# Optimization experiments

Hardware: AMD Instinct MI355X
Metric: run time of the kernel (lower is better)

Reference implementation:

```python
import jax, jax.numpy as jnp
import numpy as np

EPS = 1e-8  # torch.cosine_similarity eps


def setup_inputs() -> dict:
    key = jax.random.key(0)
    k1, k2 = jax.random.split(key)
    N, D, TOPIC_E, NT = 4096, 512, 10, 6  # NT = topic_e - topic_s + 1
    x = jax.random.normal(k1, (N, D), dtype=jnp.float32)
    # H mimics the concatenated, abs()'d H_list: (input_feature, topic_e, num_topics)
    H = jax.random.uniform(k2, (D, TOPIC_E, NT), dtype=jnp.float32)
    return {"x": x, "H": H}


def reference(x, H):
    N, D = x.shape
    num_topics = H.shape[2]

    # W_list[n, t, i] = (x @ H[:, :, i])[n, t]
    W_list = jnp.einsum('nd,dti->nti', x, H)          # (N, topic_e, num_topics)
    W_max = jnp.argmax(W_list, axis=1)                # (N, num_topics), int

    # cosine similarity matrix S[a, b] = cos(x[a], x[b]) (symmetric)
    norms = jnp.maximum(jnp.linalg.norm(x, axis=1), EPS)  # (N,)
    xn = x / norms[:, None]
    S = xn @ xn.T                                      # (N, N)

    # topic-match fraction F[a, b] = mean_k [W_max[a,k] == W_max[b,k]] (symmetric)
    comp = (W_max[:, None, :] == W_max[None, :, :])    # (N, N, num_topics) bool
    F = comp.sum(axis=2).astype(jnp.float32) / num_topics

    # C[a, b] = topic_count * sim; new_nodes[b] = mean_a C[a,b] * cat(x[b], x[a])
    C = F * S                                          # (N, N)
    col_mean = C.mean(axis=0)                          # (N,) mean over a
    out_first = x * col_mean[:, None]                  # (N, D): x[b] * mean_a C[a,b]
    out_second = (C.T @ x) / N                         # (N, D): (1/N) sum_a C[a,b] x[a]
    return jnp.concatenate([out_first, out_second], axis=1)  # (N, 2D)
```

## Files before the change

### kernel.cpp

```cpp
#include <hip/hip_runtime.h>
#include <hip/hip_bf16.h>

#define DD 512
#define NTOP 10
#define NTK 6
#define NPAIR 60

typedef float f32x4 __attribute__((ext_vector_type(4)));
typedef short bf16x8 __attribute__((ext_vector_type(8)));
typedef unsigned short us8 __attribute__((ext_vector_type(8)));
typedef unsigned short us4 __attribute__((ext_vector_type(4)));

__device__ __forceinline__ void gload16(const void* g, void* l) {
  __builtin_amdgcn_global_load_lds(
      (const __attribute__((address_space(1))) unsigned int*)g,
      (__attribute__((address_space(3))) unsigned int*)l, 16, 0, 0);
}

__global__ __launch_bounds__(256) void kern_wmax(
    const float* __restrict__ x, const float* __restrict__ H,
    int* __restrict__ codes, float* __restrict__ inv_norm,
    float* __restrict__ col_sum)
{
  __shared__ float xs[4][DD];
  __shared__ float w[4][NPAIR];
  const int wv = threadIdx.x >> 6, lane = threadIdx.x & 63;
  const int n = blockIdx.x * 4 + wv;
  const float* xr = x + (size_t)n * DD;
  float ss = 0.f;
#pragma unroll
  for (int j = 0; j < 2; ++j) {
    float4 v = *(const float4*)(xr + j * 256 + lane * 4);
    *(float4*)&xs[wv][j * 256 + lane * 4] = v;
    ss = fmaf(v.x, v.x, fmaf(v.y, v.y, fmaf(v.z, v.z, fmaf(v.w, v.w, ss))));
  }
#pragma unroll
  for (int off = 32; off; off >>= 1) ss += __shfl_xor(ss, off);
  if (lane == 0) inv_norm[n] = 1.0f / fmaxf(sqrtf(ss), 1e-8f);
  __syncthreads();
  if (lane < NPAIR) {
    float acc = 0.f;
#pragma unroll 8
    for (int d = 0; d < DD; ++d) acc = fmaf(xs[wv][d], H[d * NPAIR + lane], acc);
    w[wv][lane] = acc;
  }
  __syncthreads();
  int myc = 0;
  if (lane < NTK) {
    float best = w[wv][lane];
    int bi = 0;
#pragma unroll
    for (int t = 1; t < NTOP; ++t) {
      float v = w[wv][t * NTK + lane];
      if (v > best) { best = v; bi = t; }
    }
    myc = bi << (4 * lane);
  }
#pragma unroll
  for (int off = 1; off <= 4; off <<= 1) myc |= __shfl_xor(myc, off);
  if (lane == 0) { codes[n] = myc; col_sum[n] = 0.f; }
}

__global__ __launch_bounds__(256) void kern_prep(
    const float* __restrict__ x, const float* __restrict__ inv_norm,
    __hip_bfloat16* __restrict__ xn, __hip_bfloat16* __restrict__ xT, int N)
{
  __shared__ float tile[64][65];
  const int n0 = blockIdx.x * 64, d0 = blockIdx.y * 64;
  const int tid = threadIdx.x;
  const int r = tid >> 2, cseg = (tid & 3) * 16;
  const float* src = x + (size_t)(n0 + r) * DD + d0 + cseg;
  const float invn = inv_norm[n0 + r];
  unsigned short hb[16];
#pragma unroll
  for (int q = 0; q < 4; ++q) {
    float4 v = *(const float4*)(src + q * 4);
    tile[r][cseg + q * 4 + 0] = v.x; tile[r][cseg + q * 4 + 1] = v.y;
    tile[r][cseg + q * 4 + 2] = v.z; tile[r][cseg + q * 4 + 3] = v.w;
    hb[q * 4 + 0] = __builtin_bit_cast(unsigned short, __float2bfloat16(v.x * invn));
    hb[q * 4 + 1] = __builtin_bit_cast(unsigned short, __float2bfloat16(v.y * invn));
    hb[q * 4 + 2] = __builtin_bit_cast(unsigned short, __float2bfloat16(v.z * invn));
    hb[q * 4 + 3] = __builtin_bit_cast(unsigned short, __float2bfloat16(v.w * invn));
  }
  us8 v0, v1;
#pragma unroll
  for (int i = 0; i < 8; ++i) { v0[i] = hb[i]; v1[i] = hb[i + 8]; }
  *(us8*)(xn + (size_t)(n0 + r) * DD + d0 + cseg) = v0;
  *(us8*)(xn + (size_t)(n0 + r) * DD + d0 + cseg + 8) = v1;
  __syncthreads();
  const int drow = tid >> 2, nseg = (tid & 3) * 16;
  unsigned short hb2[16];
#pragma unroll
  for (int i = 0; i < 16; ++i)
    hb2[i] = __builtin_bit_cast(unsigned short, __float2bfloat16(tile[nseg + i][drow]));
  us8 w0, w1;
#pragma unroll
  for (int i = 0; i < 8; ++i) { w0[i] = hb2[i]; w1[i] = hb2[i + 8]; }
  *(us8*)(xT + (size_t)(d0 + drow) * N + n0 + nseg) = w0;
  *(us8*)(xT + (size_t)(d0 + drow) * N + n0 + nseg + 8) = w1;
}

#define GBM 128
#define GBK 64

__global__ __launch_bounds__(512, 4) void kern_gram(
    const __hip_bfloat16* __restrict__ xn, const int* __restrict__ codes,
    __hip_bfloat16* __restrict__ Cb, float* __restrict__ col_sum, int N)
{
  __shared__ __hip_bfloat16 lds[2 * GBM * GBK];
  __shared__ float csA[GBM], csB[GBM];
  __hip_bfloat16* As = lds;
  __hip_bfloat16* Bs = lds + GBM * GBK;
  const int tid = threadIdx.x;

  int idx = blockIdx.x, ai = 0, rem = N / GBM;
  while (idx >= rem) { idx -= rem; ++ai; --rem; }
  const int bi = ai + idx;
  const bool diag = (ai == bi);
  const int a0 = ai * GBM, b0 = bi * GBM;

  if (tid < GBM) { csA[tid] = 0.f; csB[tid] = 0.f; }

  const int lane = tid & 63, wid = tid >> 6;
  const int wr = wid >> 2, wc = wid & 3;

  const f32x4 fz = {0.f, 0.f, 0.f, 0.f};
  f32x4 acc[4][2];
#pragma unroll
  for (int m = 0; m < 4; ++m)
#pragma unroll
    for (int n = 0; n < 2; ++n) acc[m][n] = fz;

  int ldsoff[2]; size_t srcA[2], srcB[2];
#pragma unroll
  for (int i = 0; i < 2; ++i) {
    int p = i * 8192 + tid * 16;
    int row = p >> 7, c = (p >> 4) & 7;
    ldsoff[i] = p;
    size_t cc = (size_t)((c ^ (row & 7)) << 4);
    srcA[i] = (size_t)(a0 + row) * (DD * 2) + cc;
    srcB[i] = (size_t)(b0 + row) * (DD * 2) + cc;
  }
  const char* xc = (const char*)xn;

  for (int kc = 0; kc < DD * 2; kc += GBK * 2) {
#pragma unroll
    for (int i = 0; i < 2; ++i) {
      gload16(xc + srcA[i] + kc, (char*)As + ldsoff[i]);
      gload16(xc + srcB[i] + kc, (char*)Bs + ldsoff[i]);
    }
    __syncthreads();
#pragma unroll
    for (int kk = 0; kk < 2; ++kk) {
      const int kb = kk * 64 + (lane >> 4) * 16;
      bf16x8 af[4], bfr[2];
#pragma unroll
      for (int m = 0; m < 4; ++m) {
        int r = wr * 64 + m * 16 + (lane & 15);
        af[m] = *(const bf16x8*)((const char*)As + r * 128 + (kb ^ ((r & 7) << 4)));
      }
#pragma unroll
      for (int n = 0; n < 2; ++n) {
        int r = wc * 32 + n * 16 + (lane & 15);
        bfr[n] = *(const bf16x8*)((const char*)Bs + r * 128 + (kb ^ ((r & 7) << 4)));
      }
#pragma unroll
      for (int m = 0; m < 4; ++m)
#pragma unroll
        for (int n = 0; n < 2; ++n)
          acc[m][n] = __builtin_amdgcn_mfma_f32_16x16x32_bf16(af[m], bfr[n], acc[m][n], 0, 0, 0);
    }
    __syncthreads();
  }

  char* ldsb = (char*)lds;
  const int rq = (lane >> 4) << 2;
  int cb[2];
#pragma unroll
  for (int n = 0; n < 2; ++n) cb[n] = codes[b0 + wc * 32 + n * 16 + (lane & 15)];

  us4 tvs[4][2];
  float colpart[2] = {0.f, 0.f};
  float rowpart[4][4] = {};
#pragma unroll
  for (int m = 0; m < 4; ++m) {
    int ca[4];
#pragma unroll
    for (int j = 0; j < 4; ++j) ca[j] = codes[a0 + wr * 64 + m * 16 + rq + j];
#pragma unroll
    for (int n = 0; n < 2; ++n) {
      const int col = wc * 32 + n * 16 + (lane & 15);
#pragma unroll
      for (int j = 0; j < 4; ++j) {
        int t = ca[j] ^ cb[n];
        t |= t >> 1; t |= t >> 2;
        t &= 0x111111;
        float f = (float)(6 - __popc(t)) * (1.0f / 6.0f);
        float cv = acc[m][n][j] * f;
        colpart[n] += cv;
        rowpart[m][j] += cv;
        __hip_bfloat16 hv = __float2bfloat16(cv);
        tvs[m][n][j] = __builtin_bit_cast(unsigned short, hv);
        const int row = wr * 64 + m * 16 + rq + j;
        const int boff = row * 256 + ((((col >> 3) ^ (row & 7)) << 4) | ((col & 7) << 1));
        *(__hip_bfloat16*)(ldsb + boff) = hv;
      }
    }
  }
#pragma unroll
  for (int n = 0; n < 2; ++n) {
    float v = colpart[n];
    v += __shfl_xor(v, 16);
    v += __shfl_xor(v, 32);
    if (lane < 16) atomicAdd(&csB[wc * 32 + n * 16 + lane], v);
  }
  if (!diag) {
#pragma unroll
    for (int m = 0; m < 4; ++m)
#pragma unroll
      for (int j = 0; j < 4; ++j) {
        float v = rowpart[m][j];
        v += __shfl_xor(v, 1);
        v += __shfl_xor(v, 2);
        v += __shfl_xor(v, 4);
        v += __shfl_xor(v, 8);
        if ((lane & 15) == 0)
          atomicAdd(&csA[wr * 64 + m * 16 + rq + j], v);
      }
  }
  __syncthreads();
#pragma unroll
  for (int i = 0; i < 4; ++i) {
    const int row = i * 32 + (tid >> 4);
    const int ch = tid & 15;
    us8 v = *(us8*)(ldsb + row * 256 + ((ch ^ (row & 7)) << 4));
    *(us8*)((char*)Cb + ((size_t)(a0 + row) * N + b0) * 2 + (ch << 4)) = v;
  }
  if (!diag) {
    __syncthreads();
#pragma unroll
    for (int m = 0; m < 4; ++m) {
      const int row0 = wr * 64 + m * 16 + rq;
      const int chT = row0 >> 3;
      const int byo = (row0 & 7) << 1;
#pragma unroll
      for (int n = 0; n < 2; ++n) {
        const int col = wc * 32 + n * 16 + (lane & 15);
        *(us4*)(ldsb + col * 256 + (((chT ^ (col & 7)) << 4) | byo)) = tvs[m][n];
      }
    }
    __syncthreads();
#pragma unroll
    for (int i = 0; i < 4; ++i) {
      const int row = i * 32 + (tid >> 4);
      const int ch = tid & 15;
      us8 v = *(us8*)(ldsb + row * 256 + ((ch ^ (row & 7)) << 4));
      *(us8*)((char*)Cb + ((size_t)(b0 + row) * N + a0) * 2 + (ch << 4)) = v;
    }
  }
  if (tid < GBM) {
    atomicAdd(&col_sum[b0 + tid], csB[tid]);
    if (!diag) atomicAdd(&col_sum[a0 + tid], csA[tid]);
  }
}

#define OM 128
#define ON 128
#define OK 64
#define OSK 4

__global__ __launch_bounds__(512, 4) void kern_out2(
    const __hip_bfloat16* __restrict__ Cb, const __hip_bfloat16* __restrict__ xT,
    float* __restrict__ part, int N)
{
  __shared__ __hip_bfloat16 As[OM * OK];
  __shared__ __hip_bfloat16 Bs[ON * OK];
  const int tid = threadIdx.x;
  const int b0 = blockIdx.x * OM;
  const int d0 = blockIdx.y * ON;
  const int KSL = N / OSK;
  const size_t kbyte0 = (size_t)blockIdx.z * KSL * 2;
  const int lane = tid & 63, wid = tid >> 6;
  const int wr = wid >> 2, wc = wid & 3;

  const f32x4 fz = {0.f, 0.f, 0.f, 0.f};
  f32x4 acc[4][2];
#pragma unroll
  for (int m = 0; m < 4; ++m)
#pragma unroll
    for (int n = 0; n < 2; ++n) acc[m][n] = fz;

  int ldso[2]; size_t srcA[2], srcB[2];
#pragma unroll
  for (int i = 0; i < 2; ++i) {
    int p = i * 8192 + tid * 16;
    int row = p >> 7, c = (p >> 4) & 7;
    ldso[i] = p;
    size_t cc = (size_t)((c ^ (row & 7)) << 4);
    srcA[i] = (size_t)(b0 + row) * ((size_t)N * 2) + cc + kbyte0;
    srcB[i] = (size_t)(d0 + row) * ((size_t)N * 2) + cc + kbyte0;
  }
  const char* Ac = (const char*)Cb;
  const char* Bc = (const char*)xT;

  for (int kc = 0; kc < KSL * 2; kc += OK * 2) {
#pragma unroll
    for (int i = 0; i < 2; ++i) {
      gload16(Ac + srcA[i] + kc, (char*)As + ldso[i]);
      gload16(Bc + srcB[i] + kc, (char*)Bs + ldso[i]);
    }
    __syncthreads();
#pragma unroll
    for (int kk = 0; kk < 2; ++kk) {
      const int kb = kk * 64 + (lane >> 4) * 16;
      bf16x8 af[4], bfr[2];
#pragma unroll
      for (int m = 0; m < 4; ++m) {
        int r = wr * 64 + m * 16 + (lane & 15);
        af[m] = *(const bf16x8*)((const char*)As + r * 128 + (kb ^ ((r & 7) << 4)));
      }
#pragma unroll
      for (int n = 0; n < 2; ++n) {
        int r = wc * 32 + n * 16 + (lane & 15);
        bfr[n] = *(const bf16x8*)((const char*)Bs + r * 128 + (kb ^ ((r & 7) << 4)));
      }
#pragma unroll
      for (int m = 0; m < 4; ++m)
#pragma unroll
        for (int n = 0; n < 2; ++n)
          acc[m][n] = __builtin_amdgcn_mfma_f32_16x16x32_bf16(af[m], bfr[n], acc[m][n], 0, 0, 0);
    }
    __syncthreads();
  }

  float* pz = part + (size_t)blockIdx.z * N * DD;
#pragma unroll
  for (int m = 0; m < 4; ++m)
#pragma unroll
    for (int j = 0; j < 4; ++j) {
      int b = b0 + wr * 64 + m * 16 + ((lane >> 4) << 2) + j;
#pragma unroll
      for (int n = 0; n < 2; ++n) {
        int d = d0 + wc * 32 + n * 16 + (lane & 15);
        pz[(size_t)b * DD + d] = acc[m][n][j];
      }
    }
}

__global__ __launch_bounds__(256) void kern_finish(
    const float* __restrict__ x, const float* __restrict__ col_sum,
    const float* __restrict__ part, float* __restrict__ out, int N)
{
  const int n = blockIdx.x;
  const int tid = threadIdx.x;
  const float invN = 1.0f / (float)N;
  if (tid < 128) {
    const float s = col_sum[n] * invN;
    float4 v = ((const float4*)(x + (size_t)n * DD))[tid];
    v.x *= s; v.y *= s; v.z *= s; v.w *= s;
    ((float4*)(out + (size_t)n * (2 * DD)))[tid] = v;
  } else {
    const int d4 = tid - 128;
    const size_t stride = (size_t)N * DD;
    const float4* p0 = (const float4*)(part + (size_t)n * DD) + d4;
    const float4* p1 = (const float4*)(part + stride + (size_t)n * DD) + d4;
    const float4* p2 = (const float4*)(part + 2 * stride + (size_t)n * DD) + d4;
    const float4* p3 = (const float4*)(part + 3 * stride + (size_t)n * DD) + d4;
    float4 a = *p0, b = *p1, c = *p2, d = *p3;
    float4 r;
    r.x = ((a.x + b.x) + (c.x + d.x)) * invN;
    r.y = ((a.y + b.y) + (c.y + d.y)) * invN;
    r.z = ((a.z + b.z) + (c.z + d.z)) * invN;
    r.w = ((a.w + b.w) + (c.w + d.w)) * invN;
    ((float4*)(out + (size_t)n * (2 * DD) + DD))[d4] = r;
  }
}

extern "C" void kernel_launch(void* const* d_in, const int* in_sizes, int n_in,
                              void* d_out, int out_size, void* d_ws, size_t ws_size,
                              hipStream_t stream) {
  const float* x = (const float*)d_in[0];
  const float* H = (const float*)d_in[1];
  float* out = (float*)d_out;
  const int N = in_sizes[0] / DD;

  char* ws = (char*)d_ws;
  __hip_bfloat16* Cb   = (__hip_bfloat16*)ws;
  __hip_bfloat16* xn16 = (__hip_bfloat16*)(ws + (size_t)N * N * 2);
  __hip_bfloat16* xT16 = xn16 + (size_t)N * DD;
  float* part     = (float*)(xT16 + (size_t)N * DD);
  float* col_sum  = part + (size_t)4 * N * DD;
  float* inv_norm = col_sum + N;
  int*   codes    = (int*)(inv_norm + N);

  kern_wmax<<<N / 4, 256, 0, stream>>>(x, H, codes, inv_norm, col_sum);
  kern_prep<<<dim3(N / 64, DD / 64), 256, 0, stream>>>(x, inv_norm, xn16, xT16, N);
  const int T = N / GBM;
  kern_gram<<<T * (T + 1) / 2, 512, 0, stream>>>(xn16, codes, Cb, col_sum, N);
  kern_out2<<<dim3(N / OM, DD / ON, OSK), 512, 0, stream>>>(Cb, xT16, part, N);
  kern_finish<<<N, 256, 0, stream>>>(x, col_sum, part, out, N);
}
```

Before: 87.69 us.

## Widen out2 GEMM tile to 128x256 with 8-way split-K and reorder gram blocks

Adds a second C^T·x GEMM kernel that uses 128x256 output tiles, so each loaded Cb tile is reused across twice as many columns. It splits K eight ways to keep the grid large and falls back to the old 128x128, 4-way split when the workspace is too small for eight partial buffers. The gram kernel now schedules off-diagonal tiles before the cheaper diagonal tiles. The cost is twice as much partial-sum traffic in the finish kernel and more accumulator registers per thread.

```diff
diff --git a/kernel.cpp b/kernel.cpp
--- a/kernel.cpp
+++ b/kernel.cpp
@@ -113,9 +113,16 @@
   __hip_bfloat16* Bs = lds + GBM * GBK;
   const int tid = threadIdx.x;
 
-  int idx = blockIdx.x, ai = 0, rem = N / GBM;
-  while (idx >= rem) { idx -= rem; ++ai; --rem; }
-  const int bi = ai + idx;
+  const int T = N / GBM;
+  const int NOFF = T * (T - 1) / 2;
+  int ai, bi;
+  if ((int)blockIdx.x < NOFF) {
+    int idx = blockIdx.x; ai = 0; int rem = T - 1;
+    while (idx >= rem) { idx -= rem; ++ai; --rem; }
+    bi = ai + 1 + idx;
+  } else {
+    ai = bi = blockIdx.x - NOFF;
+  }
   const bool diag = (ai == bi);
   const int a0 = ai * GBM, b0 = bi * GBM;
 
@@ -264,21 +271,99 @@
   }
 }
 
-#define OM 128
-#define ON 128
-#define OK 64
-#define OSK 4
-
-__global__ __launch_bounds__(512, 4) void kern_out2(
+__global__ __launch_bounds__(512, 4) void kern_out2b(
     const __hip_bfloat16* __restrict__ Cb, const __hip_bfloat16* __restrict__ xT,
     float* __restrict__ part, int N)
 {
-  __shared__ __hip_bfloat16 As[OM * OK];
-  __shared__ __hip_bfloat16 Bs[ON * OK];
+  __shared__ __hip_bfloat16 As[128 * 64];
+  __shared__ __hip_bfloat16 Bs[256 * 64];
   const int tid = threadIdx.x;
-  const int b0 = blockIdx.x * OM;
-  const int d0 = blockIdx.y * ON;
-  const int KSL = N / OSK;
+  const int b0 = blockIdx.x * 128;
+  const int d0 = blockIdx.y * 256;
+  const int KSL = N / 8;
+  const size_t kbyte0 = (size_t)blockIdx.z * KSL * 2;
+  const int lane = tid & 63, wid = tid >> 6;
+  const int wr = wid >> 2, wc = wid & 3;
+
+  const f32x4 fz = {0.f, 0.f, 0.f, 0.f};
+  f32x4 acc[4][4];
+#pragma unroll
+  for (int m = 0; m < 4; ++m)
+#pragma unroll
+    for (int n = 0; n < 4; ++n) acc[m][n] = fz;
+
+  int ldsA[2]; size_t srcA[2];
+#pragma unroll
+  for (int i = 0; i < 2; ++i) {
+    int p = i * 8192 + tid * 16;
+    int row = p >> 7, c = (p >> 4) & 7;
+    ldsA[i] = p;
+    srcA[i] = (size_t)(b0 + row) * ((size_t)N * 2) + (size_t)((c ^ (row & 7)) << 4) + kbyte0;
+  }
+  int ldsB[4]; size_t srcB[4];
+#pragma unroll
+  for (int i = 0; i < 4; ++i) {
+    int p = i * 8192 + tid * 16;
+    int row = p >> 7, c = (p >> 4) & 7;
+    ldsB[i] = p;
+    srcB[i] = (size_t)(d0 + row) * ((size_t)N * 2) + (size_t)((c ^ (row & 7)) << 4) + kbyte0;
+  }
+  const char* Ac = (const char*)Cb;
+  const char* Bc = (const char*)xT;
+
+  for (int kc = 0; kc < KSL * 2; kc += 128) {
+#pragma unroll
+    for (int i = 0; i < 2; ++i) gload16(Ac + srcA[i] + kc, (char*)As + ldsA[i]);
+#pragma unroll
+    for (int i = 0; i < 4; ++i) gload16(Bc + srcB[i] + kc, (char*)Bs + ldsB[i]);
+    __syncthreads();
+#pragma unroll
+    for (int kk = 0; kk < 2; ++kk) {
+      const int kb = kk * 64 + (lane >> 4) * 16;
+      bf16x8 af[4], bfr[4];
+#pragma unroll
+      for (int m = 0; m < 4; ++m) {
+        int r = wr * 64 + m * 16 + (lane & 15);
+        af[m] = *(const bf16x8*)((const char*)As + r * 128 + (kb ^ ((r & 7) << 4)));
+      }
+#pragma unroll
+      for (int n = 0; n < 4; ++n) {
+        int r = wc * 64 + n * 16 + (lane & 15);
+        bfr[n] = *(const bf16x8*)((const char*)Bs + r * 128 + (kb ^ ((r & 7) << 4)));
+      }
+#pragma unroll
+      for (int m = 0; m < 4; ++m)
+#pragma unroll
+        for (int n = 0; n < 4; ++n)
+          acc[m][n] = __builtin_amdgcn_mfma_f32_16x16x32_bf16(af[m], bfr[n], acc[m][n], 0, 0, 0);
+    }
+    __syncthreads();
+  }
+
+  float* pz = part + (size_t)blockIdx.z * N * DD;
+#pragma unroll
+  for (int m = 0; m < 4; ++m)
+#pragma unroll
+    for (int j = 0; j < 4; ++j) {
+      int b = b0 + wr * 64 + m * 16 + ((lane >> 4) << 2) + j;
+#pragma unroll
+      for (int n = 0; n < 4; ++n) {
+        int d = d0 + wc * 64 + n * 16 + (lane & 15);
+        pz[(size_t)b * DD + d] = acc[m][n][j];
+      }
+    }
+}
+
+__global__ __launch_bounds__(512, 4) void kern_out2f(
+    const __hip_bfloat16* __restrict__ Cb, const __hip_bfloat16* __restrict__ xT,
+    float* __restrict__ part, int N)
+{
+  __shared__ __hip_bfloat16 As[128 * 64];
+  __shared__ __hip_bfloat16 Bs[128 * 64];
+  const int tid = threadIdx.x;
+  const int b0 = blockIdx.x * 128;
+  const int d0 = blockIdx.y * 128;
+  const int KSL = N / 4;
   const size_t kbyte0 = (size_t)blockIdx.z * KSL * 2;
   const int lane = tid & 63, wid = tid >> 6;
   const int wr = wid >> 2, wc = wid & 3;
@@ -303,7 +388,7 @@
   const char* Ac = (const char*)Cb;
   const char* Bc = (const char*)xT;
 
-  for (int kc = 0; kc < KSL * 2; kc += OK * 2) {
+  for (int kc = 0; kc < KSL * 2; kc += 128) {
 #pragma unroll
     for (int i = 0; i < 2; ++i) {
       gload16(Ac + srcA[i] + kc, (char*)As + ldso[i]);
@@ -349,7 +434,7 @@
 
 __global__ __launch_bounds__(256) void kern_finish(
     const float* __restrict__ x, const float* __restrict__ col_sum,
-    const float* __restrict__ part, float* __restrict__ out, int N)
+    const float* __restrict__ part, float* __restrict__ out, int N, int osk)
 {
   const int n = blockIdx.x;
   const int tid = threadIdx.x;
@@ -362,16 +447,12 @@
   } else {
     const int d4 = tid - 128;
     const size_t stride = (size_t)N * DD;
-    const float4* p0 = (const float4*)(part + (size_t)n * DD) + d4;
-    const float4* p1 = (const float4*)(part + stride + (size_t)n * DD) + d4;
-    const float4* p2 = (const float4*)(part + 2 * stride + (size_t)n * DD) + d4;
-    const float4* p3 = (const float4*)(part + 3 * stride + (size_t)n * DD) + d4;
-    float4 a = *p0, b = *p1, c = *p2, d = *p3;
-    float4 r;
-    r.x = ((a.x + b.x) + (c.x + d.x)) * invN;
-    r.y = ((a.y + b.y) + (c.y + d.y)) * invN;
-    r.z = ((a.z + b.z) + (c.z + d.z)) * invN;
-    r.w = ((a.w + b.w) + (c.w + d.w)) * invN;
+    float4 r = {0.f, 0.f, 0.f, 0.f};
+    for (int z = 0; z < osk; ++z) {
+      float4 p = *((const float4*)(part + (size_t)z * stride + (size_t)n * DD) + d4);
+      r.x += p.x; r.y += p.y; r.z += p.z; r.w += p.w;
+    }
+    r.x *= invN; r.y *= invN; r.z *= invN; r.w *= invN;
     ((float4*)(out + (size_t)n * (2 * DD) + DD))[d4] = r;
   }
 }
@@ -388,15 +469,23 @@
   __hip_bfloat16* Cb   = (__hip_bfloat16*)ws;
   __hip_bfloat16* xn16 = (__hip_bfloat16*)(ws + (size_t)N * N * 2);
   __hip_bfloat16* xT16 = xn16 + (size_t)N * DD;
-  float* part     = (float*)(xT16 + (size_t)N * DD);
-  float* col_sum  = part + (size_t)4 * N * DD;
+  float* col_sum  = (float*)(xT16 + (size_t)N * DD);
   float* inv_norm = col_sum + N;
   int*   codes    = (int*)(inv_norm + N);
+  float* part     = (float*)(codes + N);
+
+  const size_t base = (size_t)((char*)part - ws);
+  const bool big = ws_size >= base + (size_t)8 * N * DD * sizeof(float);
 
   kern_wmax<<<N / 4, 256, 0, stream>>>(x, H, codes, inv_norm, col_sum);
   kern_prep<<<dim3(N / 64, DD / 64), 256, 0, stream>>>(x, inv_norm, xn16, xT16, N);
   const int T = N / GBM;
   kern_gram<<<T * (T + 1) / 2, 512, 0, stream>>>(xn16, codes, Cb, col_sum, N);
-  kern_out2<<<dim3(N / OM, DD / ON, OSK), 512, 0, stream>>>(Cb, xT16, part, N);
-  kern_finish<<<N, 256, 0, stream>>>(x, col_sum, part, out, N);
-}
+  if (big) {
+    kern_out2b<<<dim3(N / 128, DD / 256, 8), 512, 0, stream>>>(Cb, xT16, part, N);
+    kern_finish<<<N, 256, 0, stream>>>(x, col_sum, part, out, N, 8);
+  } else {
+    kern_out2f<<<dim3(N / 128, DD / 128, 4), 512, 0, stream>>>(Cb, xT16, part, N);
+    kern_finish<<<N, 256, 0, stream>>>(x, col_sum, part, out, N, 4);
+  }
+}
```

Measured after the change: 91.77 us. 1.05x slower.
